# Kernel tuning notes

Hardware: AMD Instinct MI355X
Metric: run time of the kernel (lower is better)

## Reference

```python
import jax, jax.numpy as jnp
import numpy as np

B, S, D, H = 4, 1024, 1024, 16
QL, KVL = 512, 256
NOPE, ROPE, VD = 64, 32, 64
E, TOPK, FE = 8, 2, 1024  # FE = intermediate_size // expert_num
EPS = 1e-6
NEG = -1e15

def rms_norm(x, w):
    var = jnp.mean(x * x, axis=-1, keepdims=True)
    return w * (x * jax.lax.rsqrt(var + EPS))

def rotate_half(x):
    x1, x2 = jnp.split(x, 2, axis=-1)
    return jnp.concatenate([-x2, x1], axis=-1)

def rope_tables(seq_len, dim):
    inv = 1.0 / (10000.0 ** (np.arange(0, dim, 2, dtype=np.float32) / dim))
    freqs = np.arange(seq_len, dtype=np.float32)[:, None] @ inv[None, :]
    freqs = np.concatenate([freqs, freqs], axis=-1)
    return jnp.asarray(np.cos(freqs)), jnp.asarray(np.sin(freqs))

def setup_inputs():
    key = jax.random.key(0)
    ks = jax.random.split(key, 12)
    s = 0.02
    return {
        'hidden_state': jax.random.normal(ks[0], (B, S, D), jnp.float32),
        'attention_mask': jnp.ones((B, S), jnp.int32),
        'in_ln_w': jnp.ones((D,), jnp.float32),
        'post_ln_w': jnp.ones((D,), jnp.float32),
        'wq_a_w': jax.random.normal(ks[1], (QL, D)) * s,
        'wq_a_b': jnp.zeros((QL,), jnp.float32),
        'q_norm_w': jnp.ones((QL,), jnp.float32),
        'wq_b_w': jax.random.normal(ks[2], (H * (NOPE + ROPE), QL)) * s,
        'wq_b_b': jnp.zeros((H * (NOPE + ROPE),), jnp.float32),
        'wkv_a_w': jax.random.normal(ks[3], (KVL + ROPE, D)) * s,
        'wkv_a_b': jnp.zeros((KVL + ROPE,), jnp.float32),
        'kv_norm_w': jnp.ones((KVL,), jnp.float32),
        'wkv_b_w': jax.random.normal(ks[4], (H * (NOPE + VD), KVL)) * s,
        'wo_w': jax.random.normal(ks[5], (D, H * VD)) * s,
        'wo_b': jnp.zeros((D,), jnp.float32),
        'gate_w': jax.random.normal(ks[6], (E, D)) * s,
        'gate_b': jnp.zeros((E,), jnp.float32),
        'gate_proj': jax.random.normal(ks[7], (E, FE, D)) * s,
        'up_proj': jax.random.normal(ks[8], (E, FE, D)) * s,
        'down_proj': jax.random.normal(ks[9], (E, D, FE)) * s,
    }

def _forward(hidden_state, in_ln_w, post_ln_w, wq_a_w, wq_a_b, q_norm_w, wq_b_w, wq_b_b,
             wkv_a_w, wkv_a_b, kv_norm_w, wkv_b_w, wo_w, wo_b,
             gate_w, gate_b, gate_proj, up_proj, down_proj, attention_mask):
    x = rms_norm(hidden_state, in_ln_w)
    # ---- MLA ----
    q = rms_norm(x @ wq_a_w.T + wq_a_b, q_norm_w)
    q = (q @ wq_b_w.T + wq_b_b).reshape(B, S, H, NOPE + ROPE)
    q_nope, q_pe = q[..., :NOPE], q[..., NOPE:]
    kvp = x @ wkv_a_w.T + wkv_a_b
    kv, k_pe = kvp[..., :KVL], kvp[..., KVL:]
    kv = rms_norm(kv, kv_norm_w)
    cos, sin = rope_tables(S, ROPE)
    cos = cos[None, :, None, :]
    sin = sin[None, :, None, :]
    q_pe = q_pe * cos + rotate_half(q_pe) * sin            # [B,S,H,ROPE]
    k_pe = k_pe[:, :, None, :]
    k_pe = (k_pe * cos + rotate_half(k_pe) * sin)[:, :, 0]  # [B,S,ROPE]
    # kv_cache / pe_cache are filled with detached copies in the original
    kv_c = jax.lax.stop_gradient(kv)
    pe_c = jax.lax.stop_gradient(k_pe)
    wkv_b = wkv_b_w.reshape(H, NOPE + VD, KVL)
    q_abs = jnp.einsum('bshd,hdc->bshc', q_nope, wkv_b[:, :NOPE])  # cache-absorption
    scores = (jnp.einsum('bshc,btc->bsht', q_abs, kv_c)
              + jnp.einsum('bshr,btr->bsht', q_pe, pe_c)) / np.float32(np.sqrt(NOPE + ROPE))
    causal = jnp.triu(jnp.full((S, S), NEG, dtype=scores.dtype), 1)
    mask = jnp.where((attention_mask == 0)[:, None, :], NEG, causal[None])  # [B,S,S]
    scores = scores + mask[:, :, None, :]
    probs = jax.nn.softmax(scores, axis=-1)
    o = jnp.einsum('bsht,btc->bshc', probs, kv_c)
    o = jnp.einsum('bshc,hdc->bshd', o, wkv_b[:, NOPE:])
    attn = o.reshape(B, S, H * VD) @ wo_w.T + wo_b
    h = attn + hidden_state
    # ---- MoE ----
    y = rms_norm(h, post_ln_w)
    logits = y @ gate_w.T + gate_b                                   # [B,S,E]
    _, idx = jax.lax.top_k(logits, TOPK)
    sel = jnp.any(jax.nn.one_hot(idx, E, dtype=bool), axis=-2)       # [B,S,E]
    sparse = jax.nn.softmax(jnp.where(sel, logits, -jnp.inf), axis=-1)  # zeros off top-k
    g = jax.nn.silu(jnp.einsum('bsd,efd->bsef', y, gate_proj))
    u = jnp.einsum('bsd,efd->bsef', y, up_proj)
    eo = jnp.einsum('bsef,edf->bsed', g * u, down_proj)
    moe_out = jnp.einsum('bsed,bse->bsd', eo, sparse)
    out = moe_out + h
    return out, logits.reshape(-1, E)

def reference(hidden_state, attention_mask, in_ln_w, post_ln_w, wq_a_w, wq_a_b, q_norm_w,
              wq_b_w, wq_b_b, wkv_a_w, wkv_a_b, kv_norm_w, wkv_b_w, wo_w, wo_b,
              gate_w, gate_b, gate_proj, up_proj, down_proj):
    return _forward(hidden_state, in_ln_w, post_ln_w, wq_a_w, wq_a_b, q_norm_w, wq_b_w, wq_b_b,
                    wkv_a_w, wkv_a_b, kv_norm_w, wkv_b_w, wo_w, wo_b,
                    gate_w, gate_b, gate_proj, up_proj, down_proj, attention_mask)
```

## Files before the change

### kernel.cpp

```cpp
#include <hip/hip_runtime.h>
#include <math.h>

#define NB   4
#define NS   1024
#define ND   1024
#define NH   16
#define NTOK 4096
#define NFE  1024
#define ETOK_CAP 10240

#define SCL_LOG2E 0.14724445f

static constexpr size_t OFF_GWP  = 0;
static constexpr size_t OFF_TKW  = 8192;
static constexpr size_t OFF_EW   = 16384;
static constexpr size_t OFF_INT  = 26624;
static constexpr size_t OFF_X    = 45184;
static constexpr size_t OFF_QA   = 2142336;
static constexpr size_t OFF_GATE = 2142336;
static constexpr size_t OFF_UP   = 6336640;
static constexpr size_t OFF_QAB  = 8433792;
static constexpr size_t OFF_KVP  = 9482368;
static constexpr size_t OFF_KVC  = 10662016;
static constexpr size_t OFF_WA   = 11251840;
static constexpr size_t WA_WQA   = 0;
static constexpr size_t WA_WQB   = 262144;
static constexpr size_t WA_WKVA  = 655360;
static constexpr size_t WA_WO    = 802816;
static constexpr size_t OFF_ACT  = 10530944;
static constexpr size_t WS_FLOATS = 15773824;

typedef __attribute__((ext_vector_type(8))) short bf16x8_t;
typedef __attribute__((ext_vector_type(4))) float f32x4_t;

__device__ __forceinline__ unsigned pack2(float a, float b) {
  union { float f; unsigned u; } x, y; x.f = a; y.f = b;
  unsigned lo = (x.u + 0x7fffu + ((x.u >> 16) & 1u)) >> 16;
  unsigned hi = (y.u + 0x7fffu + ((y.u >> 16) & 1u)) & 0xffff0000u;
  return (lo & 0xffffu) | hi;
}
__device__ __forceinline__ unsigned short f2bfs(float f) {
  union { float f; unsigned u; } x; x.f = f;
  return (unsigned short)((x.u + 0x7fffu + ((x.u >> 16) & 1u)) >> 16);
}

__global__ __launch_bounds__(256) void conv_bf16_kernel(
    const float* __restrict__ src, unsigned short* __restrict__ dst, int n)
{
  int i = (blockIdx.x * 256 + threadIdx.x) * 8;
  if (i >= n) return;
  float4 a = *(const float4*)(src + i);
  float4 b = *(const float4*)(src + i + 4);
  uint4 o;
  o.x = pack2(a.x, a.y); o.y = pack2(a.z, a.w);
  o.z = pack2(b.x, b.y); o.w = pack2(b.z, b.w);
  *(uint4*)(dst + i) = o;
}

__global__ __launch_bounds__(256) void conv_gwp_kernel(
    const float* __restrict__ gw, const float* __restrict__ pw, float* __restrict__ gwp)
{
  int i = blockIdx.x * 256 + threadIdx.x;
  gwp[i] = gw[i] * pw[i & 1023];
}

template<int PER>
__global__ __launch_bounds__(256) void rmsnorm_bf16(
    const float* in, int istr, const float* w, unsigned short* out, int ostr)
{
  int row = blockIdx.x, t = threadIdx.x;
  const float* ip = in + (size_t)row * istr;
  float v[PER];
  float ss = 0.f;
#pragma unroll
  for (int i = 0; i < PER; i++) { v[i] = ip[t + i*256]; ss += v[i]*v[i]; }
#pragma unroll
  for (int k = 1; k < 64; k <<= 1) ss += __shfl_xor(ss, k);
  __shared__ float red[4];
  if ((t & 63) == 0) red[t >> 6] = ss;
  __syncthreads();
  float tot = red[0] + red[1] + red[2] + red[3];
  float inv = rsqrtf(tot * (1.f / (PER * 256)) + 1e-6f);
  unsigned short* op = out + (size_t)row * ostr;
#pragma unroll
  for (int i = 0; i < PER; i++) op[t + i*256] = f2bfs(v[i] * inv * w[t + i*256]);
}

__global__ __launch_bounds__(256) void rms_gate_kernel(
    const float* __restrict__ H, const float* __restrict__ pw,
    const float* __restrict__ gwp, const float* __restrict__ gb,
    unsigned short* __restrict__ ybuf, float* __restrict__ logits)
{
  __shared__ __align__(16) float ly[1024];
  __shared__ float red[4];
  int tok = blockIdx.x, t = threadIdx.x;
  float4 hv = *(const float4*)(H + (size_t)tok * ND + t * 4);
  *(float4*)&ly[t * 4] = hv;
  float ss = hv.x*hv.x + hv.y*hv.y + hv.z*hv.z + hv.w*hv.w;
#pragma unroll
  for (int k = 1; k < 64; k <<= 1) ss += __shfl_xor(ss, k);
  if ((t & 63) == 0) red[t >> 6] = ss;
  __syncthreads();
  float inv = rsqrtf((red[0] + red[1] + red[2] + red[3]) * (1.f / 1024.f) + 1e-6f);
  float4 pw4 = *(const float4*)(pw + t * 4);
  unsigned short* yb = ybuf + (size_t)tok * ND + t * 4;
  yb[0] = f2bfs((hv.x * inv) * pw4.x);
  yb[1] = f2bfs((hv.y * inv) * pw4.y);
  yb[2] = f2bfs((hv.z * inv) * pw4.z);
  yb[3] = f2bfs((hv.w * inv) * pw4.w);
  int e = t >> 5, lane = t & 31;
  const float* w = gwp + (size_t)e * ND;
  float acc = 0.f;
  for (int d = lane; d < ND; d += 32) acc += ly[d] * w[d];
#pragma unroll
  for (int k = 16; k >= 1; k >>= 1) acc += __shfl_xor(acc, k);
  if (lane == 0) logits[(size_t)tok * 8 + e] = acc * inv + gb[e];
}

#define GSTR 72

template<bool OUTBF, bool RESID>
__global__ __launch_bounds__(256) void gemm_bf16(
    const unsigned short* __restrict__ A, int lda,
    const unsigned short* __restrict__ W, int ldw,
    const float* __restrict__ bias,
    const float* __restrict__ resid,
    void* __restrict__ Cv, int ldc, int N, int K)
{
  __shared__ __align__(16) unsigned short As[128 * GSTR];
  __shared__ __align__(16) unsigned short Ws2[128 * GSTR];
  int t = threadIdx.x;
  int m0 = blockIdx.y * 128, n0 = blockIdx.x * 128;
  int lane = t & 63, w = t >> 6;
  int mw = (w >> 1) * 64, nw = (w & 1) * 64;
  int lr = lane & 15, lg = lane >> 4;

  int srowv[4], sc8v[4];
#pragma unroll
  for (int it = 0; it < 4; it++) { int c = it*256 + t; srowv[it] = c >> 3; sc8v[it] = (c & 7) * 8; }

  uint4 pa[4], pw[4];
  auto ld = [&](int k0) {
#pragma unroll
    for (int it = 0; it < 4; it++) {
      pa[it] = *(const uint4*)(A + (size_t)(m0 + srowv[it]) * lda + k0 + sc8v[it]);
      int r = n0 + srowv[it];
      pw[it] = (r < N) ? *(const uint4*)(W + (size_t)r * ldw + k0 + sc8v[it])
                       : make_uint4(0u, 0u, 0u, 0u);
    }
  };
  auto st = [&]() {
#pragma unroll
    for (int it = 0; it < 4; it++) {
      *(uint4*)&As[srowv[it] * GSTR + sc8v[it]] = pa[it];
      *(uint4*)&Ws2[srowv[it] * GSTR + sc8v[it]] = pw[it];
    }
  };

  f32x4_t acc[4][4];
#pragma unroll
  for (int i = 0; i < 4; i++)
#pragma unroll
    for (int j = 0; j < 4; j++) acc[i][j] = (f32x4_t){0.f, 0.f, 0.f, 0.f};

  ld(0); st();
  __syncthreads();
  for (int k0 = 0; ; ) {
    int kn = k0 + 64;
    if (kn < K) ld(kn);
#pragma unroll
    for (int kk = 0; kk < 2; kk++) {
      bf16x8_t af[4], wf[4];
#pragma unroll
      for (int i = 0; i < 4; i++)
        af[i] = *(const bf16x8_t*)&As[(mw + 16*i + lr) * GSTR + kk*32 + lg*8];
#pragma unroll
      for (int j = 0; j < 4; j++)
        wf[j] = *(const bf16x8_t*)&Ws2[(nw + 16*j + lr) * GSTR + kk*32 + lg*8];
#pragma unroll
      for (int i = 0; i < 4; i++)
#pragma unroll
        for (int j = 0; j < 4; j++)
          acc[i][j] = __builtin_amdgcn_mfma_f32_16x16x32_bf16(af[i], wf[j], acc[i][j], 0, 0, 0);
    }
    k0 = kn;
    if (k0 >= K) break;
    __syncthreads();
    st();
    __syncthreads();
  }
#pragma unroll
  for (int j = 0; j < 4; j++) {
    int n = n0 + nw + 16*j + lr;
    if (n < N) {
      float bv = bias[n];
#pragma unroll
      for (int i = 0; i < 4; i++) {
#pragma unroll
        for (int r = 0; r < 4; r++) {
          int m = m0 + mw + 16*i + 4*lg + r;
          size_t off = (size_t)m * ldc + n;
          float v = acc[i][j][r] + bv;
          if (RESID) v += resid[off];
          if (OUTBF) ((unsigned short*)Cv)[off] = f2bfs(v);
          else       ((float*)Cv)[off] = v;
        }
      }
    }
  }
}

__global__ __launch_bounds__(256) void rope_q_kernel(float* qbuf)
{
  int id = blockIdx.x * 256 + threadIdx.x;
  int d = id & 15;
  int h = (id >> 4) & 15;
  int sr = id >> 8;
  int s = sr & (NS - 1);
  float inv = __expf(-(float)(2 * d) * (9.210340371976184f / 32.f));
  float fr = (float)s * inv;
  float sn, cs; sincosf(fr, &sn, &cs);
  float* p = qbuf + (size_t)sr * 1536 + h * 96 + 64;
  float x1 = p[d], x2 = p[d + 16];
  p[d]      = x1 * cs - x2 * sn;
  p[d + 16] = x2 * cs + x1 * sn;
}

__global__ __launch_bounds__(256) void rope_k_kernel(const float* kvp, unsigned short* kvc)
{
  int id = blockIdx.x * 256 + threadIdx.x;
  int d = id & 15;
  int sr = id >> 4;
  int s = sr & (NS - 1);
  float inv = __expf(-(float)(2 * d) * (9.210340371976184f / 32.f));
  float fr = (float)s * inv;
  float sn, cs; sincosf(fr, &sn, &cs);
  const float* src = kvp + (size_t)sr * 288 + 256;
  unsigned short* dst = kvc + (size_t)sr * 288 + 256;
  float x1 = src[d], x2 = src[d + 16];
  dst[d]      = f2bfs(x1 * cs - x2 * sn);
  dst[d + 16] = f2bfs(x2 * cs + x1 * sn);
}

#define KSTR 296
#define QNSTR 65
#define VPAD 40
#define OSTR2 132

__global__ __launch_bounds__(256, 2) void attn_kernel(
    const float* __restrict__ qbuf,
    const unsigned short* __restrict__ kvc,
    const float* __restrict__ wkvb,
    unsigned short* __restrict__ oproj)
{
  extern __shared__ float4 smem_f4[];
  unsigned short* sm  = (unsigned short*)smem_f4;
  unsigned short* ks  = sm;
  unsigned short* vt  = sm + 9472;
  unsigned short* ps  = sm + 19712;
  float* qn           = (float*)sm;
  unsigned short* qst = sm + 8320;
  float* o_lds        = (float*)sm;

  int bx = blockIdx.x;
  int h = blockIdx.y, b = blockIdx.z;
  int t = threadIdx.x;
  int lane = t & 63, wv_ = t >> 6;
  int lrow = lane & 15, lg = lane >> 4;
  int qrow = 16 * wv_ + lrow;

  int srow[5], sc16[5];
#pragma unroll
  for (int it = 0; it < 5; it++) {
    int c = it * 256 + t;
    srow[it] = c / 36; sc16[it] = c % 36;
  }
  bool tail = (t < 128);

  for (int half = 0; half < 2; half++) {
    int qb = half ? bx : (15 - bx);
    int row0 = b * NS + qb * 64;
    __syncthreads();

    for (int idx = t; idx < 4096; idx += 256) {
      int r = idx >> 6, c = idx & 63;
      qn[r * QNSTR + c] = qbuf[(size_t)(row0 + r) * 1536 + h * 96 + c] * SCL_LOG2E;
    }
    bf16x8_t bq[9];
    {
      const float* src = qbuf + (size_t)(row0 + qrow) * 1536 + h * 96 + 64 + lg * 8;
      unsigned short* bp = (unsigned short*)&bq[8];
#pragma unroll
      for (int j = 0; j < 8; j++) bp[j] = f2bfs(src[j] * SCL_LOG2E);
    }
    __syncthreads();
    {
      int cx = t & 63, ry = t >> 6;
      float a[16][4] = {};
      const float* wb = wkvb + (size_t)h * 32768 + cx * 4;
      for (int k = 0; k < 64; k++) {
        float4 wv = *(const float4*)(wb + (size_t)k * 256);
#pragma unroll
        for (int r = 0; r < 16; r++) {
          float qv = qn[(ry * 16 + r) * QNSTR + k];
          a[r][0] += qv * wv.x; a[r][1] += qv * wv.y; a[r][2] += qv * wv.z; a[r][3] += qv * wv.w;
        }
      }
      __syncthreads();
#pragma unroll
      for (int r = 0; r < 16; r++) {
        uint2 pk; pk.x = pack2(a[r][0], a[r][1]); pk.y = pack2(a[r][2], a[r][3]);
        *(uint2*)&qst[(ry * 16 + r) * KSTR + cx * 4] = pk;
      }
    }
    __syncthreads();
#pragma unroll
    for (int kk = 0; kk < 8; kk++)
      bq[kk] = *(const bf16x8_t*)&qst[qrow * KSTR + kk * 32 + lg * 8];
    __syncthreads();

    float m_run = -1e30f, l_run = 0.f;
    f32x4_t acco[16];
#pragma unroll
    for (int n = 0; n < 16; n++) acco[n] = (f32x4_t){0.f, 0.f, 0.f, 0.f};

    uint4 pa[5];
    unsigned short vg[32];

    auto issue = [&](int kb2) {
      const unsigned short* tb = kvc + ((size_t)b * NS + kb2 * 32) * 288;
#pragma unroll
      for (int it = 0; it < 4; it++)
        pa[it] = *(const uint4*)(tb + srow[it] * 288 + sc16[it] * 8);
      if (tail) pa[4] = *(const uint4*)(tb + srow[4] * 288 + sc16[4] * 8);
      const unsigned short* vsrc = tb + t;
#pragma unroll
      for (int k = 0; k < 32; k++) vg[k] = vsrc[k * 288];
    };
    auto commit = [&]() {
#pragma unroll
      for (int it = 0; it < 5; it++) {
        if (it == 4 && !tail) continue;
        *(uint4*)&ks[srow[it] * KSTR + sc16[it] * 8] = pa[it];
      }
      unsigned wds[16];
#pragma unroll
      for (int j = 0; j < 16; j++)
        wds[j] = (unsigned)vg[2*j] | ((unsigned)vg[2*j+1] << 16);
#pragma unroll
      for (int j = 0; j < 4; j++)
        *(uint4*)&vt[t * VPAD + j * 8] =
          make_uint4(wds[4*j], wds[4*j+1], wds[4*j+2], wds[4*j+3]);
    };

    int nkb = 2 * qb + 2;
    issue(0); commit();
    __syncthreads();
    for (int kb = 0; kb < nkb; kb++) {
      bool more = (kb + 1 < nkb);
      if (more) issue(kb + 1);
      int key0 = kb * 32;
      f32x4_t s0e = {0.f,0.f,0.f,0.f}, s0o = {0.f,0.f,0.f,0.f};
      f32x4_t s1e = {0.f,0.f,0.f,0.f}, s1o = {0.f,0.f,0.f,0.f};
#pragma unroll
      for (int kk = 0; kk < 9; kk++) {
        bf16x8_t a0 = *(const bf16x8_t*)&ks[lrow * KSTR + kk*32 + lg*8];
        bf16x8_t a1 = *(const bf16x8_t*)&ks[(16 + lrow) * KSTR + kk*32 + lg*8];
        if (kk & 1) {
          s0o = __builtin_amdgcn_mfma_f32_16x16x32_bf16(a0, bq[kk], s0o, 0, 0, 0);
          s1o = __builtin_amdgcn_mfma_f32_16x16x32_bf16(a1, bq[kk], s1o, 0, 0, 0);
        } else {
          s0e = __builtin_amdgcn_mfma_f32_16x16x32_bf16(a0, bq[kk], s0e, 0, 0, 0);
          s1e = __builtin_amdgcn_mfma_f32_16x16x32_bf16(a1, bq[kk], s1e, 0, 0, 0);
        }
      }
      f32x4_t s0a = s0e + s0o, s1a = s1e + s1o;
      int qg = qb * 64 + qrow;
      float sv[8];
      if (key0 + 31 > qb * 64 + 16 * wv_) {
#pragma unroll
        for (int r = 0; r < 4; r++) {
          sv[r]     = (key0 + 4*lg + r      <= qg) ? s0a[r] : -1e30f;
          sv[4 + r] = (key0 + 16 + 4*lg + r <= qg) ? s1a[r] : -1e30f;
        }
      } else {
#pragma unroll
        for (int r = 0; r < 4; r++) { sv[r] = s0a[r]; sv[4 + r] = s1a[r]; }
      }
      float mx = sv[0];
#pragma unroll
      for (int i = 1; i < 8; i++) mx = fmaxf(mx, sv[i]);
      mx = fmaxf(mx, __shfl_xor(mx, 16));
      mx = fmaxf(mx, __shfl_xor(mx, 32));
      if (!__all(mx - m_run <= 11.0f)) {
        float mnew = fmaxf(m_run, mx);
        float al = exp2f(m_run - mnew);
        m_run = mnew;
        l_run *= al;
        float al0 = __shfl(al, 4*lg + 0);
        float al1 = __shfl(al, 4*lg + 1);
        float al2 = __shfl(al, 4*lg + 2);
        float al3 = __shfl(al, 4*lg + 3);
#pragma unroll
        for (int n = 0; n < 16; n++) {
          acco[n][0] *= al0; acco[n][1] *= al1; acco[n][2] *= al2; acco[n][3] *= al3;
        }
      }
      float sum = 0.f;
#pragma unroll
      for (int i = 0; i < 8; i++) { sv[i] = exp2f(sv[i] - m_run); sum += sv[i]; }
      sum += __shfl_xor(sum, 16);
      sum += __shfl_xor(sum, 32);
      l_run += sum;
      {
        int swz = qrow & 3;
        int g0 = lg >> 1, h0 = lg & 1;
        uint2 p0; p0.x = pack2(sv[0], sv[1]); p0.y = pack2(sv[2], sv[3]);
        uint2 p1; p1.x = pack2(sv[4], sv[5]); p1.y = pack2(sv[6], sv[7]);
        char* pr = (char*)ps + qrow * 64;
        *(uint2*)(pr + ((g0 ^ swz) * 16 + h0 * 8))       = p0;
        *(uint2*)(pr + (((2 + g0) ^ swz) * 16 + h0 * 8)) = p1;
      }
      {
        bf16x8_t ap = *(const bf16x8_t*)((char*)ps + qrow * 64 + ((lg ^ (qrow & 3)) * 16));
#pragma unroll
        for (int n = 0; n < 16; n++) {
          bf16x8_t bv = *(const bf16x8_t*)&vt[(16*n + lrow) * VPAD + lg * 8];
          acco[n] = __builtin_amdgcn_mfma_f32_16x16x32_bf16(ap, bv, acco[n], 0, 0, 0);
        }
      }
      __syncthreads();
      if (more) { commit(); __syncthreads(); }
    }
    float li = 1.f / l_run;
    float l0 = __shfl(li, 4*lg + 0);
    float l1 = __shfl(li, 4*lg + 1);
    float l2 = __shfl(li, 4*lg + 2);
    float l3 = __shfl(li, 4*lg + 3);
    int dx = t & 15, ty2 = t >> 4;
    float pr[4][4] = {};
    const float* wb2 = wkvb + (size_t)(h * 128 + 64) * 256;
#pragma unroll
    for (int p = 0; p < 2; p++) {
      __syncthreads();
#pragma unroll
      for (int n = 8*p; n < 8*p + 8; n++) {
        int fc = 16*n + lrow - 128*p;
        o_lds[(16*wv_ + 4*lg + 0) * OSTR2 + fc] = acco[n][0] * l0;
        o_lds[(16*wv_ + 4*lg + 1) * OSTR2 + fc] = acco[n][1] * l1;
        o_lds[(16*wv_ + 4*lg + 2) * OSTR2 + fc] = acco[n][2] * l2;
        o_lds[(16*wv_ + 4*lg + 3) * OSTR2 + fc] = acco[n][3] * l3;
      }
      __syncthreads();
      for (int c = 0; c < 128; c += 4) {
        float4 w0 = *(const float4*)(wb2 + (size_t)(dx*4 + 0) * 256 + 128*p + c);
        float4 w1 = *(const float4*)(wb2 + (size_t)(dx*4 + 1) * 256 + 128*p + c);
        float4 w2 = *(const float4*)(wb2 + (size_t)(dx*4 + 2) * 256 + 128*p + c);
        float4 w3 = *(const float4*)(wb2 + (size_t)(dx*4 + 3) * 256 + 128*p + c);
#pragma unroll
        for (int i = 0; i < 4; i++) {
          float4 ov = *(const float4*)&o_lds[(ty2*4 + i) * OSTR2 + c];
          pr[i][0] += ov.x*w0.x + ov.y*w0.y + ov.z*w0.z + ov.w*w0.w;
          pr[i][1] += ov.x*w1.x + ov.y*w1.y + ov.z*w1.z + ov.w*w1.w;
          pr[i][2] += ov.x*w2.x + ov.y*w2.y + ov.z*w2.z + ov.w*w2.w;
          pr[i][3] += ov.x*w3.x + ov.y*w3.y + ov.z*w3.z + ov.w*w3.w;
        }
      }
    }
#pragma unroll
    for (int i = 0; i < 4; i++)
#pragma unroll
      for (int j = 0; j < 4; j++)
        oproj[(size_t)(row0 + ty2*4 + i) * 1024 + h * 64 + dx*4 + j] = f2bfs(pr[i][j]);
  }
}

__global__ __launch_bounds__(256) void topk_kernel(
    const float* __restrict__ logits, int* __restrict__ tke,
    float* __restrict__ tkw, int* __restrict__ cnt)
{
  int tok = blockIdx.x * 256 + threadIdx.x;
  if (tok >= NTOK) return;
  float l[8];
#pragma unroll
  for (int e2 = 0; e2 < 8; e2++) l[e2] = logits[(size_t)tok * 8 + e2];
  float v0 = l[0]; int e0 = 0;
#pragma unroll
  for (int e2 = 1; e2 < 8; e2++) if (l[e2] > v0) { v0 = l[e2]; e0 = e2; }
  float v1 = -INFINITY; int e1 = 0;
#pragma unroll
  for (int e2 = 0; e2 < 8; e2++) if (e2 != e0 && l[e2] > v1) { v1 = l[e2]; e1 = e2; }
  float x = __expf(v1 - v0);
  float w0 = 1.f / (1.f + x);
  tke[tok * 2]     = e0; tke[tok * 2 + 1] = e1;
  tkw[tok * 2]     = w0; tkw[tok * 2 + 1] = 1.f - w0;
  atomicAdd(&cnt[e0], 1);
  atomicAdd(&cnt[8 + e1], 1);
}

__global__ void offsets_kernel(const int* cnt, int* base, int* pcnt)
{
  if (threadIdx.x == 0 && blockIdx.x == 0) {
    int cum = 0;
    for (int s2 = 0; s2 < 16; s2++) {
      int p = (cnt[s2] + 127) & ~127;
      base[s2] = cum; pcnt[s2] = p; cum += p;
    }
  }
}

__global__ __launch_bounds__(256) void scatter_kernel(
    const int* __restrict__ tke, const float* __restrict__ tkw,
    const int* __restrict__ base, int* cnt2,
    int* __restrict__ etok, float* __restrict__ ew)
{
  int tok = blockIdx.x * 256 + threadIdx.x;
  if (tok >= NTOK) return;
#pragma unroll
  for (int k = 0; k < 2; k++) {
    int e = tke[tok * 2 + k];
    int seg = k * 8 + e;
    int pos = atomicAdd(&cnt2[seg], 1);
    int row = base[seg] + pos;
    etok[row] = tok;
    ew[row] = tkw[tok * 2 + k];
  }
}

__global__ __launch_bounds__(256, 3) void moe_mlp1_mfma(
    const unsigned short* __restrict__ Y,
    const unsigned short* __restrict__ Gp, const unsigned short* __restrict__ Up,
    const int* __restrict__ etok, const int* __restrict__ base,
    const int* __restrict__ pcnt, unsigned short* __restrict__ act)
{
  int seg = blockIdx.z;
  if ((int)(blockIdx.y * 128) >= pcnt[seg]) return;
  int e = seg & 7;
  __shared__ __align__(16) unsigned short As[128 * GSTR];
  __shared__ __align__(16) unsigned short Gs[64 * GSTR];
  __shared__ __align__(16) unsigned short Us[64 * GSTR];
  int t = threadIdx.x;
  int row0 = base[seg] + blockIdx.y * 128;
  int n0 = blockIdx.x * 64;
  int lane = t & 63, w = t >> 6;
  int mw = (w >> 1) * 64, nw = (w & 1) * 32;
  int lr = lane & 15, lg = lane >> 4;

  int srow = t >> 3, sc8 = (t & 7) * 8;
  int tokr[4];
#pragma unroll
  for (int it = 0; it < 4; it++) tokr[it] = etok[row0 + it*32 + srow];

  uint4 pa[4], pg[2], pu[2];
  auto ld = [&](int k0) {
#pragma unroll
    for (int it = 0; it < 4; it++)
      pa[it] = (tokr[it] >= 0)
        ? *(const uint4*)(Y + (size_t)tokr[it] * ND + k0 + sc8)
        : make_uint4(0u, 0u, 0u, 0u);
#pragma unroll
    for (int it = 0; it < 2; it++) {
      int r = n0 + it*32 + srow;
      pg[it] = *(const uint4*)(Gp + ((size_t)e * NFE + r) * ND + k0 + sc8);
      pu[it] = *(const uint4*)(Up + ((size_t)e * NFE + r) * ND + k0 + sc8);
    }
  };
  auto st = [&]() {
#pragma unroll
    for (int it = 0; it < 4; it++)
      *(uint4*)&As[(it*32 + srow) * GSTR + sc8] = pa[it];
#pragma unroll
    for (int it = 0; it < 2; it++) {
      *(uint4*)&Gs[(it*32 + srow) * GSTR + sc8] = pg[it];
      *(uint4*)&Us[(it*32 + srow) * GSTR + sc8] = pu[it];
    }
  };

  f32x4_t accg[4][2], accu[4][2];
#pragma unroll
  for (int i = 0; i < 4; i++)
#pragma unroll
    for (int j = 0; j < 2; j++) {
      accg[i][j] = (f32x4_t){0.f, 0.f, 0.f, 0.f};
      accu[i][j] = (f32x4_t){0.f, 0.f, 0.f, 0.f};
    }

  ld(0); st();
  __syncthreads();
  for (int k0 = 0; ; ) {
    int kn = k0 + 64;
    if (kn < ND) ld(kn);
#pragma unroll
    for (int kk = 0; kk < 2; kk++) {
      bf16x8_t af[4], gf[2], uf[2];
#pragma unroll
      for (int i = 0; i < 4; i++)
        af[i] = *(const bf16x8_t*)&As[(mw + 16*i + lr) * GSTR + kk*32 + lg*8];
#pragma unroll
      for (int j = 0; j < 2; j++) {
        gf[j] = *(const bf16x8_t*)&Gs[(nw + 16*j + lr) * GSTR + kk*32 + lg*8];
        uf[j] = *(const bf16x8_t*)&Us[(nw + 16*j + lr) * GSTR + kk*32 + lg*8];
      }
#pragma unroll
      for (int i = 0; i < 4; i++)
#pragma unroll
        for (int j = 0; j < 2; j++) {
          accg[i][j] = __builtin_amdgcn_mfma_f32_16x16x32_bf16(af[i], gf[j], accg[i][j], 0, 0, 0);
          accu[i][j] = __builtin_amdgcn_mfma_f32_16x16x32_bf16(af[i], uf[j], accu[i][j], 0, 0, 0);
        }
    }
    k0 = kn;
    if (k0 >= ND) break;
    __syncthreads();
    st();
    __syncthreads();
  }
#pragma unroll
  for (int i = 0; i < 4; i++)
#pragma unroll
    for (int j = 0; j < 2; j++) {
      int n = n0 + nw + 16*j + lr;
#pragma unroll
      for (int r = 0; r < 4; r++) {
        int m = row0 + mw + 16*i + 4*lg + r;
        float g = accg[i][j][r], u = accu[i][j][r];
        float s = g / (1.f + __expf(-g));
        act[(size_t)m * NFE + n] = f2bfs(s * u);
      }
    }
}

__global__ __launch_bounds__(256) void moe_down_mfma(
    const unsigned short* __restrict__ act, const unsigned short* __restrict__ Dp,
    const int* __restrict__ etok, const float* __restrict__ ew,
    const int* __restrict__ base, const int* __restrict__ pcnt,
    int slot, float* __restrict__ out)
{
  int e = blockIdx.z;
  int seg = slot * 8 + e;
  if ((int)(blockIdx.y * 128) >= pcnt[seg]) return;
  __shared__ __align__(16) unsigned short As[128 * GSTR];
  __shared__ __align__(16) unsigned short Ws2[128 * GSTR];
  int t = threadIdx.x;
  int row0 = base[seg] + blockIdx.y * 128;
  int n0 = blockIdx.x * 128;
  int lane = t & 63, w = t >> 6;
  int mw = (w >> 1) * 64, nw = (w & 1) * 64;
  int lr = lane & 15, lg = lane >> 4;

  int srowv[4], sc8v[4];
#pragma unroll
  for (int it = 0; it < 4; it++) { int c = it*256 + t; srowv[it] = c >> 3; sc8v[it] = (c & 7) * 8; }

  uint4 pa[4], pw[4];
  auto ld = [&](int k0) {
#pragma unroll
    for (int it = 0; it < 4; it++) {
      pa[it] = *(const uint4*)(act + (size_t)(row0 + srowv[it]) * NFE + k0 + sc8v[it]);
      pw[it] = *(const uint4*)(Dp + ((size_t)e * ND + n0 + srowv[it]) * NFE + k0 + sc8v[it]);
    }
  };
  auto st = [&]() {
#pragma unroll
    for (int it = 0; it < 4; it++) {
      *(uint4*)&As[srowv[it] * GSTR + sc8v[it]] = pa[it];
      *(uint4*)&Ws2[srowv[it] * GSTR + sc8v[it]] = pw[it];
    }
  };

  f32x4_t acc[4][4];
#pragma unroll
  for (int i = 0; i < 4; i++)
#pragma unroll
    for (int j = 0; j < 4; j++) acc[i][j] = (f32x4_t){0.f, 0.f, 0.f, 0.f};

  ld(0); st();
  __syncthreads();
  for (int k0 = 0; ; ) {
    int kn = k0 + 64;
    if (kn < NFE) ld(kn);
#pragma unroll
    for (int kk = 0; kk < 2; kk++) {
      bf16x8_t af[4], wf[4];
#pragma unroll
      for (int i = 0; i < 4; i++)
        af[i] = *(const bf16x8_t*)&As[(mw + 16*i + lr) * GSTR + kk*32 + lg*8];
#pragma unroll
      for (int j = 0; j < 4; j++)
        wf[j] = *(const bf16x8_t*)&Ws2[(nw + 16*j + lr) * GSTR + kk*32 + lg*8];
#pragma unroll
      for (int i = 0; i < 4; i++)
#pragma unroll
        for (int j = 0; j < 4; j++)
          acc[i][j] = __builtin_amdgcn_mfma_f32_16x16x32_bf16(af[i], wf[j], acc[i][j], 0, 0, 0);
    }
    k0 = kn;
    if (k0 >= NFE) break;
    __syncthreads();
    st();
    __syncthreads();
  }
#pragma unroll
  for (int i = 0; i < 4; i++) {
    int tks[4]; float ews[4];
#pragma unroll
    for (int r = 0; r < 4; r++) {
      int rg = row0 + mw + 16*i + 4*lg + r;
      tks[r] = etok[rg]; ews[r] = ew[rg];
    }
#pragma unroll
    for (int j = 0; j < 4; j++) {
      int n = n0 + nw + 16*j + lr;
#pragma unroll
      for (int r = 0; r < 4; r++) {
        if (tks[r] >= 0)
          out[(size_t)tks[r] * ND + n] += ews[r] * acc[i][j][r];
      }
    }
  }
}

extern "C" void kernel_launch(void* const* d_in, const int* in_sizes, int n_in,
                              void* d_out, int out_size, void* d_ws, size_t ws_size,
                              hipStream_t stream) {
  const float* hidden    = (const float*)d_in[0];
  const float* in_ln_w   = (const float*)d_in[2];
  const float* post_ln_w = (const float*)d_in[3];
  const float* wq_a_w    = (const float*)d_in[4];
  const float* wq_a_b    = (const float*)d_in[5];
  const float* q_norm_w  = (const float*)d_in[6];
  const float* wq_b_w    = (const float*)d_in[7];
  const float* wq_b_b    = (const float*)d_in[8];
  const float* wkv_a_w   = (const float*)d_in[9];
  const float* wkv_a_b   = (const float*)d_in[10];
  const float* kv_norm_w = (const float*)d_in[11];
  const float* wkv_b_w   = (const float*)d_in[12];
  const float* wo_w      = (const float*)d_in[13];
  const float* wo_b      = (const float*)d_in[14];
  const float* gate_w    = (const float*)d_in[15];
  const float* gate_b    = (const float*)d_in[16];
  const float* gate_proj = (const float*)d_in[17];
  const float* up_proj   = (const float*)d_in[18];
  const float* down_proj = (const float*)d_in[19];

  float* ws = (float*)d_ws;
  if (ws_size < WS_FLOATS * sizeof(float)) return;

  float* gwp = ws + OFF_GWP;
  float* tkw = ws + OFF_TKW;
  float* ew  = ws + OFF_EW;
  int* ib   = (int*)(ws + OFF_INT);
  int* tke  = ib;
  int* etok = ib + 8192;
  int* cnt  = ib + 8192 + ETOK_CAP;
  int* cnt2 = cnt + 16;
  int* base = cnt + 32;
  int* pcnt = cnt + 48;

  unsigned short* x_bf   = (unsigned short*)(ws + OFF_X);
  unsigned short* oproj  = (unsigned short*)(ws + OFF_X);
  unsigned short* ybuf   = (unsigned short*)(ws + OFF_X);
  float*          qa     = ws + OFF_QA;
  float*          qbuf   = ws + OFF_QA;
  unsigned short* gate_bf= (unsigned short*)(ws + OFF_GATE);
  unsigned short* down_bf= (unsigned short*)(ws + OFF_GATE);
  unsigned short* up_bf  = (unsigned short*)(ws + OFF_UP);
  unsigned short* qab    = (unsigned short*)(ws + OFF_QAB);
  float*          kvp    = ws + OFF_KVP;
  unsigned short* kvc    = (unsigned short*)(ws + OFF_KVC);
  unsigned short* actb   = (unsigned short*)(ws + OFF_ACT);
  unsigned short* wqa_bf = (unsigned short*)(ws + OFF_WA + WA_WQA);
  unsigned short* wqb_bf = (unsigned short*)(ws + OFF_WA + WA_WQB);
  unsigned short* wkva_bf= (unsigned short*)(ws + OFF_WA + WA_WKVA);
  unsigned short* wo_bf  = (unsigned short*)(ws + OFF_WA + WA_WO);

  float* out    = (float*)d_out;
  float* logits = out + (size_t)NTOK * ND;

  conv_bf16_kernel<<<256, 256, 0, stream>>>(wq_a_w, wqa_bf, 524288);
  conv_bf16_kernel<<<144, 256, 0, stream>>>(wkv_a_w, wkva_bf, 294912);
  conv_bf16_kernel<<<384, 256, 0, stream>>>(wq_b_w, wqb_bf, 786432);
  conv_bf16_kernel<<<512, 256, 0, stream>>>(wo_w, wo_bf, 1048576);
  conv_gwp_kernel<<<32, 256, 0, stream>>>(gate_w, post_ln_w, gwp);

  rmsnorm_bf16<4><<<NTOK, 256, 0, stream>>>(hidden, ND, in_ln_w, x_bf, ND);
  gemm_bf16<false,false><<<dim3(4, 32), 256, 0, stream>>>(
      x_bf, ND, wqa_bf, ND, wq_a_b, nullptr, qa, 512, 512, ND);
  gemm_bf16<false,false><<<dim3(3, 32), 256, 0, stream>>>(
      x_bf, ND, wkva_bf, ND, wkv_a_b, nullptr, kvp, 288, 288, ND);
  rmsnorm_bf16<2><<<NTOK, 256, 0, stream>>>(qa, 512, q_norm_w, qab, 512);
  rmsnorm_bf16<1><<<NTOK, 256, 0, stream>>>(kvp, 288, kv_norm_w, kvc, 288);
  gemm_bf16<false,false><<<dim3(12, 32), 256, 0, stream>>>(
      qab, 512, wqb_bf, 512, wq_b_b, nullptr, qbuf, 1536, 1536, 512);
  rope_q_kernel<<<4096, 256, 0, stream>>>(qbuf);
  rope_k_kernel<<<256, 256, 0, stream>>>(kvp, kvc);
  {
    size_t smem = 54528;
    hipFuncSetAttribute((const void*)attn_kernel,
                        hipFuncAttributeMaxDynamicSharedMemorySize, (int)smem);
    attn_kernel<<<dim3(8, NH, NB), 256, smem, stream>>>(qbuf, kvc, wkv_b_w, oproj);
  }
  conv_bf16_kernel<<<4096, 256, 0, stream>>>(gate_proj, gate_bf, 8388608);
  conv_bf16_kernel<<<4096, 256, 0, stream>>>(up_proj, up_bf, 8388608);
  gemm_bf16<false,true><<<dim3(8, 32), 256, 0, stream>>>(
      oproj, ND, wo_bf, ND, wo_b, hidden, out, ND, ND, ND);
  rms_gate_kernel<<<NTOK, 256, 0, stream>>>(out, post_ln_w, gwp, gate_b, ybuf, logits);
  hipMemsetAsync(cnt, 0, 32 * sizeof(int), stream);
  hipMemsetAsync(etok, 0xFF, ETOK_CAP * sizeof(int), stream);
  topk_kernel<<<16, 256, 0, stream>>>(logits, tke, tkw, cnt);
  offsets_kernel<<<1, 64, 0, stream>>>(cnt, base, pcnt);
  scatter_kernel<<<16, 256, 0, stream>>>(tke, tkw, base, cnt2, etok, ew);
  moe_mlp1_mfma<<<dim3(16, 32, 16), 256, 0, stream>>>(ybuf, gate_bf, up_bf,
                                                      etok, base, pcnt, actb);
  conv_bf16_kernel<<<4096, 256, 0, stream>>>(down_proj, down_bf, 8388608);
  moe_down_mfma<<<dim3(8, 32, 8), 256, 0, stream>>>(actb, down_bf, etok, ew,
                                                    base, pcnt, 0, out);
  moe_down_mfma<<<dim3(8, 32, 8), 256, 0, stream>>>(actb, down_bf, etok, ew,
                                                    base, pcnt, 1, out);
}
```

Before: 909.5 us.

## Double-buffer K/V tiles in attention and pass P via shuffles instead of LDS

```diff
diff --git a/kernel.cpp b/kernel.cpp
--- a/kernel.cpp
+++ b/kernel.cpp
@@ -256,8 +256,7 @@
   extern __shared__ float4 smem_f4[];
   unsigned short* sm  = (unsigned short*)smem_f4;
   unsigned short* ks  = sm;
-  unsigned short* vt  = sm + 9472;
-  unsigned short* ps  = sm + 19712;
+  unsigned short* vt  = sm + 18944;
   float* qn           = (float*)sm;
   unsigned short* qst = sm + 8320;
   float* o_lds        = (float*)sm;
@@ -269,6 +268,9 @@
   int lrow = lane & 15, lg = lane >> 4;
   int qrow = 16 * wv_ + lrow;
 
+  int sA = lrow + 16 * ((2 * lg) & 3);
+  int sB = sA + 16;
+
   int srow[5], sc16[5];
 #pragma unroll
   for (int it = 0; it < 5; it++) {
@@ -337,11 +339,13 @@
 #pragma unroll
       for (int k = 0; k < 32; k++) vg[k] = vsrc[k * 288];
     };
-    auto commit = [&]() {
+    auto commit = [&](int par) {
+      unsigned short* ksb = ks + par * 9472;
+      unsigned short* vtb = vt + par * 10240;
 #pragma unroll
       for (int it = 0; it < 5; it++) {
         if (it == 4 && !tail) continue;
-        *(uint4*)&ks[srow[it] * KSTR + sc16[it] * 8] = pa[it];
+        *(uint4*)&ksb[srow[it] * KSTR + sc16[it] * 8] = pa[it];
       }
       unsigned wds[16];
 #pragma unroll
@@ -349,23 +353,29 @@
         wds[j] = (unsigned)vg[2*j] | ((unsigned)vg[2*j+1] << 16);
 #pragma unroll
       for (int j = 0; j < 4; j++)
-        *(uint4*)&vt[t * VPAD + j * 8] =
+        *(uint4*)&vtb[t * VPAD + j * 8] =
           make_uint4(wds[4*j], wds[4*j+1], wds[4*j+2], wds[4*j+3]);
     };
 
     int nkb = 2 * qb + 2;
-    issue(0); commit();
+    issue(0); commit(0);
+    issue(1);
     __syncthreads();
     for (int kb = 0; kb < nkb; kb++) {
-      bool more = (kb + 1 < nkb);
-      if (more) issue(kb + 1);
+      int cur = kb & 1;
+      if (kb + 1 < nkb) {
+        commit(cur ^ 1);
+        if (kb + 2 < nkb) issue(kb + 2);
+      }
+      const unsigned short* ksb = ks + cur * 9472;
+      const unsigned short* vtb = vt + cur * 10240;
       int key0 = kb * 32;
       f32x4_t s0e = {0.f,0.f,0.f,0.f}, s0o = {0.f,0.f,0.f,0.f};
       f32x4_t s1e = {0.f,0.f,0.f,0.f}, s1o = {0.f,0.f,0.f,0.f};
 #pragma unroll
       for (int kk = 0; kk < 9; kk++) {
-        bf16x8_t a0 = *(const bf16x8_t*)&ks[lrow * KSTR + kk*32 + lg*8];
-        bf16x8_t a1 = *(const bf16x8_t*)&ks[(16 + lrow) * KSTR + kk*32 + lg*8];
+        bf16x8_t a0 = *(const bf16x8_t*)&ksb[lrow * KSTR + kk*32 + lg*8];
+        bf16x8_t a1 = *(const bf16x8_t*)&ksb[(16 + lrow) * KSTR + kk*32 + lg*8];
         if (kk & 1) {
           s0o = __builtin_amdgcn_mfma_f32_16x16x32_bf16(a0, bq[kk], s0o, 0, 0, 0);
           s1o = __builtin_amdgcn_mfma_f32_16x16x32_bf16(a1, bq[kk], s1o, 0, 0, 0);
@@ -412,25 +422,29 @@
       sum += __shfl_xor(sum, 16);
       sum += __shfl_xor(sum, 32);
       l_run += sum;
+      bf16x8_t ap;
       {
-        int swz = qrow & 3;
-        int g0 = lg >> 1, h0 = lg & 1;
-        uint2 p0; p0.x = pack2(sv[0], sv[1]); p0.y = pack2(sv[2], sv[3]);
-        uint2 p1; p1.x = pack2(sv[4], sv[5]); p1.y = pack2(sv[6], sv[7]);
-        char* pr = (char*)ps + qrow * 64;
-        *(uint2*)(pr + ((g0 ^ swz) * 16 + h0 * 8))       = p0;
-        *(uint2*)(pr + (((2 + g0) ^ swz) * 16 + h0 * 8)) = p1;
-      }
-      {
-        bf16x8_t ap = *(const bf16x8_t*)((char*)ps + qrow * 64 + ((lg ^ (qrow & 3)) * 16));
-#pragma unroll
-        for (int n = 0; n < 16; n++) {
-          bf16x8_t bv = *(const bf16x8_t*)&vt[(16*n + lrow) * VPAD + lg * 8];
-          acco[n] = __builtin_amdgcn_mfma_f32_16x16x32_bf16(ap, bv, acco[n], 0, 0, 0);
-        }
+        unsigned w0 = pack2(sv[0], sv[1]);
+        unsigned w1 = pack2(sv[2], sv[3]);
+        unsigned w2 = pack2(sv[4], sv[5]);
+        unsigned w3 = pack2(sv[6], sv[7]);
+        unsigned lo0 = __shfl(w0, sA), hi0 = __shfl(w2, sA);
+        unsigned lo1 = __shfl(w1, sA), hi1 = __shfl(w3, sA);
+        unsigned lo2 = __shfl(w0, sB), hi2 = __shfl(w2, sB);
+        unsigned lo3 = __shfl(w1, sB), hi3 = __shfl(w3, sB);
+        union { unsigned u[4]; bf16x8_t v; } apu;
+        apu.u[0] = (lg < 2) ? lo0 : hi0;
+        apu.u[1] = (lg < 2) ? lo1 : hi1;
+        apu.u[2] = (lg < 2) ? lo2 : hi2;
+        apu.u[3] = (lg < 2) ? lo3 : hi3;
+        ap = apu.v;
+      }
+#pragma unroll
+      for (int n = 0; n < 16; n++) {
+        bf16x8_t bv = *(const bf16x8_t*)&vtb[(16*n + lrow) * VPAD + lg * 8];
+        acco[n] = __builtin_amdgcn_mfma_f32_16x16x32_bf16(ap, bv, acco[n], 0, 0, 0);
       }
       __syncthreads();
-      if (more) { commit(); __syncthreads(); }
     }
     float li = 1.f / l_run;
     float l0 = __shfl(li, 4*lg + 0);
@@ -795,7 +809,7 @@
   rope_q_kernel<<<4096, 256, 0, stream>>>(qbuf);
   rope_k_kernel<<<256, 256, 0, stream>>>(kvp, kvc);
   {
-    size_t smem = 54528;
+    size_t smem = 78848;
     hipFuncSetAttribute((const void*)attn_kernel,
                         hipFuncAttributeMaxDynamicSharedMemorySize, (int)smem);
     attn_kernel<<<dim3(8, NH, NB), 256, smem, stream>>>(qbuf, kvc, wkv_b_w, oproj);
```

New measurement: 911.1 us. About the same (+0.2%).
